# Optimization experiments

Hardware: AMD Instinct MI355X
Metric: run time of the kernel (lower is better)

The kernel has to match this reference:

```python
import jax, jax.numpy as jnp
import numpy as np

PRIME = 2147483647  # 2^31 - 1, MinHash modulus
GAMMA = 0.3
NUM_HEADS = 8


def minhash_sketch(ids, a, b):
    # ids: (B, L, S) int64 atom ids; a,b: (K,) hash coefficients
    # h[b,l,s,k] = (a[k]*id + b[k]) mod PRIME ; signature = min over the set axis S
    h = (ids[..., None] * a + b) % PRIME          # (B, L, S, K)
    return h.min(axis=2)                          # (B, L, K)


def jaccard_from_signatures(sig_q, sig_k):
    # sig_q: (B, Lq, K), sig_k: (B, Lk, K) -> (B, Lq, Lk) fraction of matching slots.
    # Scan over the K hash slots to avoid materializing a (B,Lq,Lk,K) tensor.
    B, Lq, K = sig_q.shape
    Lk = sig_k.shape[1]

    def step(acc, cols):
        qc, kc = cols                              # (B,Lq), (B,Lk)
        return acc + (qc[:, :, None] == kc[:, None, :]).astype(jnp.float32), None

    init = jnp.zeros((B, Lq, Lk), jnp.float32)
    xs = (jnp.moveaxis(sig_q, -1, 0), jnp.moveaxis(sig_k, -1, 0))
    acc, _ = jax.lax.scan(step, init, xs)
    return acc / K


def symdiff_from_jaccard(jacc, size_q, size_k):
    # |A ∩ B| = J/(1+J) * (|A|+|B|)  =>  |A Δ B| = (|A|+|B|) * (1-J)/(1+J)
    tot = size_q[:, :, None] + size_k[:, None, :]   # (B, Lq, Lk)
    return tot * (1.0 - jacc) / (1.0 + jacc)


def setup_inputs() -> dict:
    key = jax.random.key(0)
    ks = jax.random.split(key, 12)
    B, Lq, Lk, E, S, K, V = 4, 1024, 1024, 512, 8, 128, 32000
    w = lambda k: (jax.random.normal(k, (E, E), jnp.float32) * 0.02)
    return {
        "query": jax.random.normal(ks[0], (B, Lq, E), jnp.float32),
        "key": jax.random.normal(ks[1], (B, Lk, E), jnp.float32),
        "value": jax.random.normal(ks[2], (B, Lk, E), jnp.float32),
        "token_sets_q": jax.random.randint(ks[3], (B, Lq, S), 0, V).astype(jnp.int64),
        "token_sets_k": jax.random.randint(ks[4], (B, Lk, S), 0, V).astype(jnp.int64),
        "hash_a": jax.random.randint(ks[5], (K,), 1, PRIME - 1).astype(jnp.int64),
        "hash_b": jax.random.randint(ks[6], (K,), 0, PRIME - 1).astype(jnp.int64),
        "Wq": w(ks[7]), "bq": jnp.zeros((E,), jnp.float32),
        "Wk": w(ks[8]), "bk": jnp.zeros((E,), jnp.float32),
        "Wv": w(ks[9]), "bv": jnp.zeros((E,), jnp.float32),
        "Wo": w(ks[10]), "bo": jnp.zeros((E,), jnp.float32),
    }


def reference(query, key, value, token_sets_q, token_sets_k, hash_a, hash_b,
              Wq, bq, Wk, bk, Wv, bv, Wo, bo):
    B, Lq, E = query.shape
    Lk = key.shape[1]
    H = NUM_HEADS
    d = E // H

    # in-projections (torch Linear: x @ W^T + b); q,k are computed but the
    # attention scores come solely from the token-set kernel (gating disabled)
    q = query @ Wq.T + bq
    k = key @ Wk.T + bk
    v = (value @ Wv.T + bv).reshape(B, Lk, H, d).transpose(0, 2, 1, 3)  # (B,H,Lk,d)

    # MinHash sketches of per-token atom sets -> estimated Jaccard -> Δ-RBF score
    sig_q = minhash_sketch(token_sets_q, hash_a, hash_b)   # (B,Lq,K)
    sig_k = minhash_sketch(token_sets_k, hash_a, hash_b)   # (B,Lk,K)
    jacc = jaccard_from_signatures(sig_q, sig_k)           # (B,Lq,Lk)

    S = token_sets_q.shape[-1]
    size_q = jnp.full((B, Lq), S, jnp.float32)             # uniform CSR offsets -> |set| = S
    size_k = jnp.full((B, Lk), S, jnp.float32)
    delta = symdiff_from_jaccard(jacc, size_q, size_k)
    scores = jnp.exp(-GAMMA * delta)                       # (B,Lq,Lk), shared by all heads

    attn = jax.nn.softmax(scores, axis=-1)                 # no masks, no causal, dropout=0
    ctx = jnp.einsum('bqk,bhkd->bqhd', attn, v).reshape(B, Lq, E)
    return ctx @ Wo.T + bo
```

## Files before the change

### kernel.cpp

```cpp
#include <hip/hip_runtime.h>
#include <hip/hip_bf16.h>
#include <stdint.h>

#define PRIME 2147483647u
#define GAMMA 0.3f
#define K_HASH 128
#define S_SET 8
#define NB 4
#define LQ 1024
#define LK 1024
#define EDIM 512

typedef unsigned short ushort_t;
typedef __attribute__((ext_vector_type(8))) short short8;
typedef __attribute__((ext_vector_type(4))) float f32x4;

static __device__ __forceinline__ unsigned short f2bf(float f) {
    unsigned u = __builtin_bit_cast(unsigned, f);
    u += 0x7FFFu + ((u >> 16) & 1u);
    return (unsigned short)(u >> 16);
}

static __device__ __forceinline__ void glds16(const void* g, void* l) {
    __builtin_amdgcn_global_load_lds(
        (const __attribute__((address_space(1))) unsigned int*)g,
        (__attribute__((address_space(3))) unsigned int*)l, 16, 0, 0);
}

#define SWZ(r) ((((r) >> 2) & 3) ^ ((r) & 3))

static __device__ __forceinline__ float score_of(int m) {
    float r = (float)(K_HASH - m) / (float)(K_HASH + m);
    return expf(expf(-GAMMA * (2.0f * S_SET) * r));
}

template<int SEPI>
static __device__ void gemm64_dev(
        const ushort_t* __restrict__ A, const ushort_t* __restrict__ B,
        ushort_t* __restrict__ C, float* __restrict__ Sacc,
        int lda, int ldb, int ldc, int Kd, int m0, int n0,
        ushort_t* AsBase, ushort_t* BsBase, int tid) {
    ushort_t (*As)[64 * 32] = (ushort_t (*)[64 * 32])AsBase;
    ushort_t (*Bs)[64 * 32] = (ushort_t (*)[64 * 32])BsBase;
    int w = tid >> 6, lane = tid & 63;
    int wm = (w & 1) * 32, wn = (w >> 1) * 32;
    int mrow = lane & 15, kg = lane >> 4;

    int r = tid >> 2, c = (tid & 3) ^ SWZ(r);
    const ushort_t* pa = A + (size_t)(m0 + r) * lda + c * 8;
    const ushort_t* pb = B + (size_t)(n0 + r) * ldb + c * 8;

    int aoff[2], boff[2];
    #pragma unroll
    for (int s = 0; s < 2; s++) {
        int Ra = wm + s * 16 + mrow;
        aoff[s] = Ra * 32 + (kg ^ SWZ(Ra)) * 8;
        int Rb = wn + s * 16 + mrow;
        boff[s] = Rb * 32 + (kg ^ SWZ(Rb)) * 8;
    }

    f32x4 acc[2][2] = {};
    int nK = Kd >> 5;
    glds16(pa, &As[0][tid * 8]);
    glds16(pb, &Bs[0][tid * 8]);
    for (int i = 0; i < nK; i++) {
        __syncthreads();
        int cur = i & 1, nxt = cur ^ 1;
        if (i + 1 < nK) {
            int k0 = (i + 1) << 5;
            glds16(pa + k0, &As[nxt][tid * 8]);
            glds16(pb + k0, &Bs[nxt][tid * 8]);
        }
        short8 af[2], bh[2];
        #pragma unroll
        for (int s = 0; s < 2; s++) {
            af[s] = *(const short8*)&As[cur][aoff[s]];
            bh[s] = *(const short8*)&Bs[cur][boff[s]];
        }
        #pragma unroll
        for (int ii = 0; ii < 2; ii++)
            #pragma unroll
            for (int jj = 0; jj < 2; jj++)
                acc[ii][jj] = __builtin_amdgcn_mfma_f32_16x16x32_bf16(
                                  af[ii], bh[jj], acc[ii][jj], 0, 0, 0);
    }

    int col = lane & 15, rbase = (lane >> 4) * 4;
    #pragma unroll
    for (int ii = 0; ii < 2; ii++) {
        #pragma unroll
        for (int jj = 0; jj < 2; jj++) {
            #pragma unroll
            for (int rr = 0; rr < 4; rr++) {
                int gm = m0 + wm + ii * 16 + rbase + rr;
                int gn = n0 + wn + jj * 16 + col;
                C[(size_t)gm * ldc + gn] = f2bf(acc[ii][jj][rr]);
            }
        }
    }
    if (SEPI) {
        #pragma unroll
        for (int jj = 0; jj < 2; jj++) {
            float s = 0.f;
            #pragma unroll
            for (int ii = 0; ii < 2; ii++)
                #pragma unroll
                for (int rr = 0; rr < 4; rr++) s += acc[ii][jj][rr];
            s += __shfl_xor(s, 16);
            s += __shfl_xor(s, 32);
            if ((lane >> 4) == 0)
                atomicAdd(&Sacc[(m0 >> 10) * EDIM + n0 + wn + jj * 16 + col], s);
        }
    }
}

#define BOB_BLOCKS 8
#define SZ_BLOCKS 1
#define CVT_N0 (NB * LK * EDIM)
#define CVT_N1 (EDIM * EDIM)
#define CVT_BLOCKS ((CVT_N0 + CVT_N1) / (256 * 8))
#define MZ_BLOCKS 1024
#define SIGT_BLOCKS 128
#define WVT_BLOCKS 64
#define PREP_GRID (BOB_BLOCKS + SZ_BLOCKS + CVT_BLOCKS + MZ_BLOCKS + SIGT_BLOCKS + WVT_BLOCKS)

__global__ __launch_bounds__(256) void prep_kernel(
        const float* __restrict__ value, const float* __restrict__ Wv,
        const float* __restrict__ Wo, const float* __restrict__ bv,
        const float* __restrict__ bo,
        ushort_t* __restrict__ Vb, ushort_t* __restrict__ Wob,
        ushort_t* __restrict__ WvT,
        const int* __restrict__ ts_q, const int* __restrict__ ts_k,
        const int* __restrict__ ha, const int* __restrict__ hb,
        unsigned* __restrict__ sigTq, unsigned* __restrict__ sigTk,
        uint8_t* __restrict__ M, float* __restrict__ S,
        float* __restrict__ bob) {
    __shared__ unsigned tile[128 * 65];
    __shared__ int ids_s[64 * S_SET];
    int blk = blockIdx.x, tid = threadIdx.x;
    if (blk < BOB_BLOCKS) {
        int w = tid >> 6, lane = tid & 63;
        #pragma unroll
        for (int i = 0; i < 16; i++) {
            int row = blk * 64 + w * 16 + i;
            const float* wr = Wo + (size_t)row * EDIM;
            float s = 0.f;
            #pragma unroll
            for (int c2 = 0; c2 < 8; c2++)
                s += bv[lane + 64 * c2] * wr[lane + 64 * c2];
            #pragma unroll
            for (int off = 32; off; off >>= 1) s += __shfl_down(s, off);
            if (lane == 0) bob[row] = bo[row] + s;
        }
        return;
    }
    if (blk < BOB_BLOCKS + SZ_BLOCKS) {
        ((float2*)S)[tid] = (float2){0.f, 0.f};
        ((float2*)S)[256 + tid] = (float2){0.f, 0.f};
        ((float2*)S)[512 + tid] = (float2){0.f, 0.f};
        ((float2*)S)[768 + tid] = (float2){0.f, 0.f};
        return;
    }
    if (blk < BOB_BLOCKS + SZ_BLOCKS + CVT_BLOCKS) {
        size_t i = ((size_t)(blk - BOB_BLOCKS - SZ_BLOCKS) * 256 + tid) * 8;
        const float* src; ushort_t* dst; size_t off;
        if (i < CVT_N0) { src = value; dst = Vb;  off = i; }
        else            { src = Wo;    dst = Wob; off = i - CVT_N0; }
        float4 a = *(const float4*)(src + off);
        float4 b = *(const float4*)(src + off + 4);
        ushort4 o0, o1;
        o0.x = f2bf(a.x); o0.y = f2bf(a.y); o0.z = f2bf(a.z); o0.w = f2bf(a.w);
        o1.x = f2bf(b.x); o1.y = f2bf(b.y); o1.z = f2bf(b.z); o1.w = f2bf(b.w);
        *(ushort4*)(dst + off)     = o0;
        *(ushort4*)(dst + off + 4) = o1;
        return;
    }
    if (blk < BOB_BLOCKS + SZ_BLOCKS + CVT_BLOCKS + MZ_BLOCKS) {
        size_t off = ((size_t)(blk - BOB_BLOCKS - SZ_BLOCKS - CVT_BLOCKS) * 256 + tid) * 16;
        *(int4*)(M + off) = (int4){0, 0, 0, 0};
        return;
    }
    if (blk < BOB_BLOCKS + SZ_BLOCKS + CVT_BLOCKS + MZ_BLOCKS + SIGT_BLOCKS) {
        int sb = blk - (BOB_BLOCKS + SZ_BLOCKS + CVT_BLOCKS + MZ_BLOCKS);
        int r0 = sb * 64;
        const int* ts = (r0 < NB * LQ) ? ts_q : ts_k;
        unsigned* sigT = (r0 < NB * LQ) ? sigTq : sigTk;
        int base = r0 & (NB * LQ - 1);
        ((int2*)ids_s)[tid] = ((const int2*)(ts + (size_t)base * S_SET))[tid];
        __syncthreads();
        int kt = tid & 127, rt = tid >> 7;
        unsigned long long a  = (unsigned)ha[kt];
        unsigned long long bb = (unsigned)hb[kt];
        for (int r = rt; r < 64; r += 2) {
            unsigned mn = 0xFFFFFFFFu;
            #pragma unroll
            for (int s = 0; s < S_SET; s++) {
                unsigned long long x =
                    a * (unsigned long long)(unsigned)ids_s[r * S_SET + s] + bb;
                x = (x & PRIME) + (x >> 31);
                x = (x & PRIME) + (x >> 31);
                unsigned rr = (unsigned)x;
                if (rr >= PRIME) rr -= PRIME;
                mn = (rr < mn) ? rr : mn;
            }
            tile[kt * 65 + r] = mn;
        }
        __syncthreads();
        #pragma unroll
        for (int ch = 0; ch < 32; ch++) {
            int idx = ch * 256 + tid;
            int k = idx >> 6, r = idx & 63;
            sigT[(size_t)k * (NB * LQ) + base + r] = tile[k * 65 + r];
        }
        return;
    }
    int wt = blk - (BOB_BLOCKS + SZ_BLOCKS + CVT_BLOCKS + MZ_BLOCKS + SIGT_BLOCKS);
    int r0 = (wt >> 3) * 64, c0 = (wt & 7) * 64;
    ushort_t (*tt)[65] = (ushort_t (*)[65])tile;
    #pragma unroll
    for (int p = 0; p < 16; p++) {
        int idx = p * 256 + tid, r = idx >> 6, c = idx & 63;
        tt[c][r] = f2bf(Wv[(size_t)(r0 + r) * EDIM + c0 + c]);
    }
    __syncthreads();
    #pragma unroll
    for (int p = 0; p < 16; p++) {
        int idx = p * 256 + tid, r = idx >> 6, c = idx & 63;
        WvT[(size_t)(c0 + r) * EDIM + r0 + c] = tt[r][c];
    }
}

union JSmem {
    struct { unsigned keys[2048]; ushort_t vals[2048]; } j;
    struct { ushort_t As[2][64 * 32]; ushort_t Bs[2][64 * 32]; } g;
};

__global__ __launch_bounds__(256) void joing1_kernel(
        const unsigned* __restrict__ sigTq, const unsigned* __restrict__ sigTk,
        uint8_t* __restrict__ M,
        const ushort_t* __restrict__ Wob, const ushort_t* __restrict__ WvT,
        ushort_t* __restrict__ Wvo) {
    __shared__ JSmem sm;
    int blk = blockIdx.x, tid = threadIdx.x;
    if (blk < 64) {
        gemm64_dev<0>(Wob, WvT, Wvo, nullptr,
                      EDIM, EDIM, EDIM, EDIM,
                      (blk >> 3) * 64, (blk & 7) * 64,
                      sm.g.As[0], sm.g.Bs[0], tid);
        return;
    }
    int jt = blk - 64, b = jt >> 7, k = jt & 127;
    const unsigned* kc = sigTk + (size_t)k * (NB * LK) + b * LK;
    const unsigned* qc = sigTq + (size_t)k * (NB * LQ) + b * LQ;
    uint4 kv = ((const uint4*)kc)[tid];
    uint4 qv = ((const uint4*)qc)[tid];
    #pragma unroll
    for (int i = 0; i < 8; i++) sm.j.keys[i * 256 + tid] = 0xFFFFFFFFu;
    __syncthreads();
    unsigned vvv[4] = {kv.x, kv.y, kv.z, kv.w};
    unsigned hh[4]; bool dn[4];
    #pragma unroll
    for (int e = 0; e < 4; e++) { hh[e] = (vvv[e] * 2654435761u) >> 21; dn[e] = false; }
    int rem = 4;
    while (rem) {
        #pragma unroll
        for (int e = 0; e < 4; e++) {
            if (dn[e]) continue;
            unsigned prev = atomicCAS(&sm.j.keys[hh[e]], 0xFFFFFFFFu, vvv[e]);
            if (prev == 0xFFFFFFFFu) {
                sm.j.vals[hh[e]] = (ushort_t)(tid * 4 + e);
                dn[e] = true; rem--;
            } else hh[e] = (hh[e] + 1) & 2047;
        }
    }
    __syncthreads();
    uint8_t* Mb = M + ((size_t)b << 20);
    unsigned qq[4] = {qv.x, qv.y, qv.z, qv.w};
    #pragma unroll
    for (int e = 0; e < 4; e++) { hh[e] = (qq[e] * 2654435761u) >> 21; dn[e] = false; }
    rem = 4;
    while (rem) {
        unsigned kk[4];
        #pragma unroll
        for (int e = 0; e < 4; e++) kk[e] = sm.j.keys[hh[e]];
        #pragma unroll
        for (int e = 0; e < 4; e++) {
            if (dn[e]) continue;
            if (kk[e] == 0xFFFFFFFFu) { dn[e] = true; rem--; }
            else {
                if (kk[e] == qq[e]) {
                    unsigned ix = ((unsigned)(tid * 4 + e) << 10) + sm.j.vals[hh[e]];
                    atomicAdd((unsigned*)(Mb + (ix & ~3u)), 1u << ((ix & 3u) * 8));
                }
                hh[e] = (hh[e] + 1) & 2047;
            }
        }
    }
}

__global__ __launch_bounds__(256) void g2_kernel(
        const ushort_t* __restrict__ Vb, const ushort_t* __restrict__ Wvo,
        ushort_t* __restrict__ W2c, float* __restrict__ S) {
    __shared__ ushort_t As[2][64 * 32], Bs[2][64 * 32];
    int blk = blockIdx.x;
    gemm64_dev<1>(Vb, Wvo, W2c, S,
                  EDIM, EDIM, EDIM, EDIM,
                  (blk >> 3) * 64, (blk & 7) * 64,
                  As[0], Bs[0], threadIdx.x);
}

__global__ __launch_bounds__(256) void outk_kernel(
        const uint8_t* __restrict__ M, const ushort_t* __restrict__ W2c,
        const float* __restrict__ S, const float* __restrict__ bob,
        float* __restrict__ out) {
    __shared__ unsigned lj[256];
    __shared__ float lp[256];
    __shared__ unsigned lcnt;
    int row = blockIdx.x, tid = threadIdx.x, b = row >> 10;
    const uint8_t* Mr = M + ((size_t)row << 10);
    float p0 = score_of(0);
    float acc0 = 0.f, acc1 = 0.f, drs = 0.f;
    int n0 = tid * 2;
    for (int c = 0; c < 4; c++) {
        if (tid == 0) lcnt = 0;
        __syncthreads();
        uint8_t m = Mr[c * 256 + tid];
        if (m) {
            unsigned s = atomicAdd(&lcnt, 1u);
            lj[s] = c * 256 + tid;
            lp[s] = score_of((int)m) - p0;
        }
        __syncthreads();
        unsigned cnt = lcnt;
        for (unsigned i = 0; i < cnt; i++) {
            float w = lp[i];
            drs += w;
            const ushort_t* wr = W2c + (((size_t)(b << 10) + lj[i]) << 9);
            unsigned pk = *(const unsigned*)(wr + n0);
            acc0 += w * __builtin_bit_cast(float, pk << 16);
            acc1 += w * __builtin_bit_cast(float, pk & 0xFFFF0000u);
        }
        __syncthreads();
    }
    float rs = 1024.0f * p0 + drs;
    float inv = 1.0f / rs;
    float2 sv = *(const float2*)(S + b * EDIM + n0);
    float2 bb = *(const float2*)(bob + n0);
    float2 o;
    o.x = (p0 * sv.x + acc0) * inv + bb.x;
    o.y = (p0 * sv.y + acc1) * inv + bb.y;
    *(float2*)(out + (size_t)row * EDIM + n0) = o;
}

extern "C" void kernel_launch(void* const* d_in, const int* in_sizes, int n_in,
                              void* d_out, int out_size, void* d_ws, size_t ws_size,
                              hipStream_t stream) {
    const float* value = (const float*)d_in[2];
    const int* tsq = (const int*)d_in[3];
    const int* tsk = (const int*)d_in[4];
    const int* ha  = (const int*)d_in[5];
    const int* hb  = (const int*)d_in[6];
    const float* Wv = (const float*)d_in[11];
    const float* bv = (const float*)d_in[12];
    const float* Wo = (const float*)d_in[13];
    const float* bo = (const float*)d_in[14];
    float* out = (float*)d_out;

    char* ws = (char*)d_ws;
    unsigned* sigTq = (unsigned*)(ws);
    unsigned* sigTk = (unsigned*)(ws + (2ull << 20));
    uint8_t*  M     = (uint8_t*)(ws + (4ull << 20));
    ushort_t* Vb    = (ushort_t*)(ws + (8ull << 20));
    ushort_t* W2c   = (ushort_t*)(ws + (12ull << 20));
    ushort_t* Wob   = (ushort_t*)(ws + (16ull << 20));
    ushort_t* WvT   = (ushort_t*)(ws + (16ull << 20) + (512ull << 10));
    ushort_t* Wvo   = (ushort_t*)(ws + (17ull << 20));
    float* S        = (float*)(ws + (17ull << 20) + (512ull << 10));
    float* bob      = (float*)(ws + (17ull << 20) + (520ull << 10));

    prep_kernel<<<PREP_GRID, 256, 0, stream>>>(
        value, Wv, Wo, bv, bo, Vb, Wob, WvT,
        tsq, tsk, ha, hb, sigTq, sigTk, M, S, bob);

    joing1_kernel<<<576, 256, 0, stream>>>(
        sigTq, sigTk, M, Wob, WvT, Wvo);

    g2_kernel<<<512, 256, 0, stream>>>(Vb, Wvo, W2c, S);

    outk_kernel<<<NB * LQ, 256, 0, stream>>>(M, W2c, S, bob, out);
}
```

Before: 161.2 us.

## Fuse four kernels into one cooperative persistent kernel with grid syncs

Merges the prep, join/GEMM1, GEMM2 and output kernels into a single 512-block cooperative kernel that runs four phases separated by grid-wide syncs, with a fallback to four separate launches if the cooperative launch fails. Work in each phase is redistributed over 512 persistent blocks (grid-stride loops for conversion/zeroing, multiple rows per block in the output phase). The goal is to remove launch overhead and inter-kernel gaps, at the cost of grid-sync latency, a larger shared-memory union, and less parallelism in the output phase (512 blocks instead of 4096).

```diff
diff --git a/kernel.cpp b/kernel.cpp
--- a/kernel.cpp
+++ b/kernel.cpp
@@ -1,6 +1,9 @@
 #include <hip/hip_runtime.h>
 #include <hip/hip_bf16.h>
+#include <hip/hip_cooperative_groups.h>
 #include <stdint.h>
+
+namespace cg = cooperative_groups;
 
 #define PRIME 2147483647u
 #define GAMMA 0.3f
@@ -33,6 +36,13 @@
     float r = (float)(K_HASH - m) / (float)(K_HASH + m);
     return expf(expf(-GAMMA * (2.0f * S_SET) * r));
 }
+
+union FSmem {
+    struct { unsigned tile[128 * 65]; int ids[64 * S_SET]; } t;
+    struct { unsigned keys[2048]; ushort_t vals[2048]; } j;
+    struct { ushort_t As[2][64 * 32]; ushort_t Bs[2][64 * 32]; } g;
+    struct { unsigned lj[256]; float lp[256]; unsigned lcnt; } o;
+};
 
 template<int SEPI>
 static __device__ void gemm64_dev(
@@ -114,242 +124,232 @@
     }
 }
 
-#define BOB_BLOCKS 8
-#define SZ_BLOCKS 1
 #define CVT_N0 (NB * LK * EDIM)
 #define CVT_N1 (EDIM * EDIM)
-#define CVT_BLOCKS ((CVT_N0 + CVT_N1) / (256 * 8))
-#define MZ_BLOCKS 1024
-#define SIGT_BLOCKS 128
-#define WVT_BLOCKS 64
-#define PREP_GRID (BOB_BLOCKS + SZ_BLOCKS + CVT_BLOCKS + MZ_BLOCKS + SIGT_BLOCKS + WVT_BLOCKS)
-
-__global__ __launch_bounds__(256) void prep_kernel(
+#define CVT_U ((CVT_N0 + CVT_N1) / 8)
+#define MZ_U (NB * LQ * LK / 16)
+#define TOT_U (CVT_U + MZ_U)
+
+__global__ __launch_bounds__(256, 2) void fused_kernel(
         const float* __restrict__ value, const float* __restrict__ Wv,
         const float* __restrict__ Wo, const float* __restrict__ bv,
         const float* __restrict__ bo,
-        ushort_t* __restrict__ Vb, ushort_t* __restrict__ Wob,
-        ushort_t* __restrict__ WvT,
         const int* __restrict__ ts_q, const int* __restrict__ ts_k,
         const int* __restrict__ ha, const int* __restrict__ hb,
         unsigned* __restrict__ sigTq, unsigned* __restrict__ sigTk,
-        uint8_t* __restrict__ M, float* __restrict__ S,
-        float* __restrict__ bob) {
-    __shared__ unsigned tile[128 * 65];
-    __shared__ int ids_s[64 * S_SET];
+        uint8_t* __restrict__ M,
+        ushort_t* __restrict__ Vb, ushort_t* __restrict__ Wob,
+        ushort_t* __restrict__ WvT, ushort_t* __restrict__ Wvo,
+        ushort_t* __restrict__ W2c, float* __restrict__ S,
+        float* __restrict__ bob, float* __restrict__ out,
+        int plo, int phi) {
+    __shared__ FSmem sm;
     int blk = blockIdx.x, tid = threadIdx.x;
-    if (blk < BOB_BLOCKS) {
-        int w = tid >> 6, lane = tid & 63;
-        #pragma unroll
-        for (int i = 0; i < 16; i++) {
-            int row = blk * 64 + w * 16 + i;
-            const float* wr = Wo + (size_t)row * EDIM;
-            float s = 0.f;
-            #pragma unroll
-            for (int c2 = 0; c2 < 8; c2++)
-                s += bv[lane + 64 * c2] * wr[lane + 64 * c2];
-            #pragma unroll
-            for (int off = 32; off; off >>= 1) s += __shfl_down(s, off);
-            if (lane == 0) bob[row] = bo[row] + s;
-        }
-        return;
-    }
-    if (blk < BOB_BLOCKS + SZ_BLOCKS) {
-        ((float2*)S)[tid] = (float2){0.f, 0.f};
-        ((float2*)S)[256 + tid] = (float2){0.f, 0.f};
-        ((float2*)S)[512 + tid] = (float2){0.f, 0.f};
-        ((float2*)S)[768 + tid] = (float2){0.f, 0.f};
-        return;
-    }
-    if (blk < BOB_BLOCKS + SZ_BLOCKS + CVT_BLOCKS) {
-        size_t i = ((size_t)(blk - BOB_BLOCKS - SZ_BLOCKS) * 256 + tid) * 8;
-        const float* src; ushort_t* dst; size_t off;
-        if (i < CVT_N0) { src = value; dst = Vb;  off = i; }
-        else            { src = Wo;    dst = Wob; off = i - CVT_N0; }
-        float4 a = *(const float4*)(src + off);
-        float4 b = *(const float4*)(src + off + 4);
-        ushort4 o0, o1;
-        o0.x = f2bf(a.x); o0.y = f2bf(a.y); o0.z = f2bf(a.z); o0.w = f2bf(a.w);
-        o1.x = f2bf(b.x); o1.y = f2bf(b.y); o1.z = f2bf(b.z); o1.w = f2bf(b.w);
-        *(ushort4*)(dst + off)     = o0;
-        *(ushort4*)(dst + off + 4) = o1;
-        return;
-    }
-    if (blk < BOB_BLOCKS + SZ_BLOCKS + CVT_BLOCKS + MZ_BLOCKS) {
-        size_t off = ((size_t)(blk - BOB_BLOCKS - SZ_BLOCKS - CVT_BLOCKS) * 256 + tid) * 16;
-        *(int4*)(M + off) = (int4){0, 0, 0, 0};
-        return;
-    }
-    if (blk < BOB_BLOCKS + SZ_BLOCKS + CVT_BLOCKS + MZ_BLOCKS + SIGT_BLOCKS) {
-        int sb = blk - (BOB_BLOCKS + SZ_BLOCKS + CVT_BLOCKS + MZ_BLOCKS);
-        int r0 = sb * 64;
-        const int* ts = (r0 < NB * LQ) ? ts_q : ts_k;
-        unsigned* sigT = (r0 < NB * LQ) ? sigTq : sigTk;
-        int base = r0 & (NB * LQ - 1);
-        ((int2*)ids_s)[tid] = ((const int2*)(ts + (size_t)base * S_SET))[tid];
-        __syncthreads();
-        int kt = tid & 127, rt = tid >> 7;
-        unsigned long long a  = (unsigned)ha[kt];
-        unsigned long long bb = (unsigned)hb[kt];
-        for (int r = rt; r < 64; r += 2) {
-            unsigned mn = 0xFFFFFFFFu;
-            #pragma unroll
-            for (int s = 0; s < S_SET; s++) {
-                unsigned long long x =
-                    a * (unsigned long long)(unsigned)ids_s[r * S_SET + s] + bb;
-                x = (x & PRIME) + (x >> 31);
-                x = (x & PRIME) + (x >> 31);
-                unsigned rr = (unsigned)x;
-                if (rr >= PRIME) rr -= PRIME;
-                mn = (rr < mn) ? rr : mn;
+
+    for (int ph = plo; ph <= phi; ph++) {
+        if (ph == 0) {
+            if (blk < 128) {
+                int r0 = blk * 64;
+                const int* ts = (r0 < NB * LQ) ? ts_q : ts_k;
+                unsigned* sigT = (r0 < NB * LQ) ? sigTq : sigTk;
+                int base = r0 & (NB * LQ - 1);
+                ((int2*)sm.t.ids)[tid] =
+                    ((const int2*)(ts + (size_t)base * S_SET))[tid];
+                __syncthreads();
+                int kt = tid & 127, rt = tid >> 7;
+                unsigned long long a  = (unsigned)ha[kt];
+                unsigned long long bb = (unsigned)hb[kt];
+                for (int r = rt; r < 64; r += 2) {
+                    unsigned mn = 0xFFFFFFFFu;
+                    #pragma unroll
+                    for (int s = 0; s < S_SET; s++) {
+                        unsigned long long x =
+                            a * (unsigned long long)(unsigned)sm.t.ids[r * S_SET + s] + bb;
+                        x = (x & PRIME) + (x >> 31);
+                        x = (x & PRIME) + (x >> 31);
+                        unsigned rr = (unsigned)x;
+                        if (rr >= PRIME) rr -= PRIME;
+                        mn = (rr < mn) ? rr : mn;
+                    }
+                    sm.t.tile[kt * 65 + r] = mn;
+                }
+                __syncthreads();
+                #pragma unroll
+                for (int ch = 0; ch < 32; ch++) {
+                    int idx = ch * 256 + tid;
+                    int k = idx >> 6, r = idx & 63;
+                    sigT[(size_t)k * (NB * LQ) + base + r] = sm.t.tile[k * 65 + r];
+                }
+            } else if (blk < 136) {
+                int w = tid >> 6, lane = tid & 63;
+                #pragma unroll
+                for (int i = 0; i < 16; i++) {
+                    int row = (blk - 128) * 64 + w * 16 + i;
+                    const float* wr = Wo + (size_t)row * EDIM;
+                    float s = 0.f;
+                    #pragma unroll
+                    for (int c2 = 0; c2 < 8; c2++)
+                        s += bv[lane + 64 * c2] * wr[lane + 64 * c2];
+                    #pragma unroll
+                    for (int off = 32; off; off >>= 1) s += __shfl_down(s, off);
+                    if (lane == 0) bob[row] = bo[row] + s;
+                }
+            } else if (blk == 136) {
+                #pragma unroll
+                for (int i = 0; i < 4; i++)
+                    ((float4*)S)[i * 256 + tid] = (float4){0.f, 0.f, 0.f, 0.f};
+            } else if (blk < 201) {
+                int wt = blk - 137;
+                int r0 = (wt >> 3) * 64, c0 = (wt & 7) * 64;
+                ushort_t (*tt)[65] = (ushort_t (*)[65])sm.t.tile;
+                #pragma unroll
+                for (int p = 0; p < 16; p++) {
+                    int idx = p * 256 + tid, r = idx >> 6, c = idx & 63;
+                    tt[c][r] = f2bf(Wv[(size_t)(r0 + r) * EDIM + c0 + c]);
+                }
+                __syncthreads();
+                #pragma unroll
+                for (int p = 0; p < 16; p++) {
+                    int idx = p * 256 + tid, r = idx >> 6, c = idx & 63;
+                    WvT[(size_t)(c0 + r) * EDIM + r0 + c] = tt[r][c];
+                }
+            } else {
+                for (size_t u = (size_t)(blk - 201) * 256 + tid; u < TOT_U;
+                     u += (size_t)311 * 256) {
+                    if (u < CVT_U) {
+                        size_t i = u * 8;
+                        const float* src; ushort_t* dst; size_t off;
+                        if (i < CVT_N0) { src = value; dst = Vb;  off = i; }
+                        else            { src = Wo;    dst = Wob; off = i - CVT_N0; }
+                        float4 a = *(const float4*)(src + off);
+                        float4 b = *(const float4*)(src + off + 4);
+                        ushort4 o0, o1;
+                        o0.x = f2bf(a.x); o0.y = f2bf(a.y);
+                        o0.z = f2bf(a.z); o0.w = f2bf(a.w);
+                        o1.x = f2bf(b.x); o1.y = f2bf(b.y);
+                        o1.z = f2bf(b.z); o1.w = f2bf(b.w);
+                        *(ushort4*)(dst + off)     = o0;
+                        *(ushort4*)(dst + off + 4) = o1;
+                    } else {
+                        *(int4*)(M + (u - CVT_U) * 16) = (int4){0, 0, 0, 0};
+                    }
+                }
             }
-            tile[kt * 65 + r] = mn;
-        }
-        __syncthreads();
-        #pragma unroll
-        for (int ch = 0; ch < 32; ch++) {
-            int idx = ch * 256 + tid;
-            int k = idx >> 6, r = idx & 63;
-            sigT[(size_t)k * (NB * LQ) + base + r] = tile[k * 65 + r];
-        }
-        return;
-    }
-    int wt = blk - (BOB_BLOCKS + SZ_BLOCKS + CVT_BLOCKS + MZ_BLOCKS + SIGT_BLOCKS);
-    int r0 = (wt >> 3) * 64, c0 = (wt & 7) * 64;
-    ushort_t (*tt)[65] = (ushort_t (*)[65])tile;
-    #pragma unroll
-    for (int p = 0; p < 16; p++) {
-        int idx = p * 256 + tid, r = idx >> 6, c = idx & 63;
-        tt[c][r] = f2bf(Wv[(size_t)(r0 + r) * EDIM + c0 + c]);
-    }
-    __syncthreads();
-    #pragma unroll
-    for (int p = 0; p < 16; p++) {
-        int idx = p * 256 + tid, r = idx >> 6, c = idx & 63;
-        WvT[(size_t)(c0 + r) * EDIM + r0 + c] = tt[r][c];
-    }
-}
-
-union JSmem {
-    struct { unsigned keys[2048]; ushort_t vals[2048]; } j;
-    struct { ushort_t As[2][64 * 32]; ushort_t Bs[2][64 * 32]; } g;
-};
-
-__global__ __launch_bounds__(256) void joing1_kernel(
-        const unsigned* __restrict__ sigTq, const unsigned* __restrict__ sigTk,
-        uint8_t* __restrict__ M,
-        const ushort_t* __restrict__ Wob, const ushort_t* __restrict__ WvT,
-        ushort_t* __restrict__ Wvo) {
-    __shared__ JSmem sm;
-    int blk = blockIdx.x, tid = threadIdx.x;
-    if (blk < 64) {
-        gemm64_dev<0>(Wob, WvT, Wvo, nullptr,
-                      EDIM, EDIM, EDIM, EDIM,
-                      (blk >> 3) * 64, (blk & 7) * 64,
-                      sm.g.As[0], sm.g.Bs[0], tid);
-        return;
-    }
-    int jt = blk - 64, b = jt >> 7, k = jt & 127;
-    const unsigned* kc = sigTk + (size_t)k * (NB * LK) + b * LK;
-    const unsigned* qc = sigTq + (size_t)k * (NB * LQ) + b * LQ;
-    uint4 kv = ((const uint4*)kc)[tid];
-    uint4 qv = ((const uint4*)qc)[tid];
-    #pragma unroll
-    for (int i = 0; i < 8; i++) sm.j.keys[i * 256 + tid] = 0xFFFFFFFFu;
-    __syncthreads();
-    unsigned vvv[4] = {kv.x, kv.y, kv.z, kv.w};
-    unsigned hh[4]; bool dn[4];
-    #pragma unroll
-    for (int e = 0; e < 4; e++) { hh[e] = (vvv[e] * 2654435761u) >> 21; dn[e] = false; }
-    int rem = 4;
-    while (rem) {
-        #pragma unroll
-        for (int e = 0; e < 4; e++) {
-            if (dn[e]) continue;
-            unsigned prev = atomicCAS(&sm.j.keys[hh[e]], 0xFFFFFFFFu, vvv[e]);
-            if (prev == 0xFFFFFFFFu) {
-                sm.j.vals[hh[e]] = (ushort_t)(tid * 4 + e);
-                dn[e] = true; rem--;
-            } else hh[e] = (hh[e] + 1) & 2047;
-        }
-    }
-    __syncthreads();
-    uint8_t* Mb = M + ((size_t)b << 20);
-    unsigned qq[4] = {qv.x, qv.y, qv.z, qv.w};
-    #pragma unroll
-    for (int e = 0; e < 4; e++) { hh[e] = (qq[e] * 2654435761u) >> 21; dn[e] = false; }
-    rem = 4;
-    while (rem) {
-        unsigned kk[4];
-        #pragma unroll
-        for (int e = 0; e < 4; e++) kk[e] = sm.j.keys[hh[e]];
-        #pragma unroll
-        for (int e = 0; e < 4; e++) {
-            if (dn[e]) continue;
-            if (kk[e] == 0xFFFFFFFFu) { dn[e] = true; rem--; }
-            else {
-                if (kk[e] == qq[e]) {
-                    unsigned ix = ((unsigned)(tid * 4 + e) << 10) + sm.j.vals[hh[e]];
-                    atomicAdd((unsigned*)(Mb + (ix & ~3u)), 1u << ((ix & 3u) * 8));
-                }
-                hh[e] = (hh[e] + 1) & 2047;
+        } else if (ph == 1) {
+            if (blk < 64) {
+                gemm64_dev<0>(Wob, WvT, Wvo, nullptr,
+                              EDIM, EDIM, EDIM, EDIM,
+                              (blk >> 3) * 64, (blk & 7) * 64,
+                              sm.g.As[0], sm.g.Bs[0], tid);
+            } else {
+                for (int u = blk - 64; u < 512; u += 448) {
+                    __syncthreads();
+                    int b = u >> 7, k = u & 127;
+                    const unsigned* kc = sigTk + (size_t)k * (NB * LK) + b * LK;
+                    const unsigned* qc = sigTq + (size_t)k * (NB * LQ) + b * LQ;
+                    uint4 kv = ((const uint4*)kc)[tid];
+                    uint4 qv = ((const uint4*)qc)[tid];
+                    #pragma unroll
+                    for (int i = 0; i < 8; i++)
+                        sm.j.keys[i * 256 + tid] = 0xFFFFFFFFu;
+                    __syncthreads();
+                    unsigned vvv[4] = {kv.x, kv.y, kv.z, kv.w};
+                    unsigned hh[4]; bool dn[4];
+                    #pragma unroll
+                    for (int e = 0; e < 4; e++) {
+                        hh[e] = (vvv[e] * 2654435761u) >> 21; dn[e] = false;
+                    }
+                    int rem = 4;
+                    while (rem) {
+                        #pragma unroll
+                        for (int e = 0; e < 4; e++) {
+                            if (dn[e]) continue;
+                            unsigned prev =
+                                atomicCAS(&sm.j.keys[hh[e]], 0xFFFFFFFFu, vvv[e]);
+                            if (prev == 0xFFFFFFFFu) {
+                                sm.j.vals[hh[e]] = (ushort_t)(tid * 4 + e);
+                                dn[e] = true; rem--;
+                            } else hh[e] = (hh[e] + 1) & 2047;
+                        }
+                    }
+                    __syncthreads();
+                    uint8_t* Mb = M + ((size_t)b << 20);
+                    unsigned qq[4] = {qv.x, qv.y, qv.z, qv.w};
+                    #pragma unroll
+                    for (int e = 0; e < 4; e++) {
+                        hh[e] = (qq[e] * 2654435761u) >> 21; dn[e] = false;
+                    }
+                    rem = 4;
+                    while (rem) {
+                        unsigned kk[4];
+                        #pragma unroll
+                        for (int e = 0; e < 4; e++) kk[e] = sm.j.keys[hh[e]];
+                        #pragma unroll
+                        for (int e = 0; e < 4; e++) {
+                            if (dn[e]) continue;
+                            if (kk[e] == 0xFFFFFFFFu) { dn[e] = true; rem--; }
+                            else {
+                                if (kk[e] == qq[e]) {
+                                    unsigned ix = ((unsigned)(tid * 4 + e) << 10)
+                                                  + sm.j.vals[hh[e]];
+                                    atomicAdd((unsigned*)(Mb + (ix & ~3u)),
+                                              1u << ((ix & 3u) * 8));
+                                }
+                                hh[e] = (hh[e] + 1) & 2047;
+                            }
+                        }
+                    }
+                }
             }
-        }
-    }
-}
-
-__global__ __launch_bounds__(256) void g2_kernel(
-        const ushort_t* __restrict__ Vb, const ushort_t* __restrict__ Wvo,
-        ushort_t* __restrict__ W2c, float* __restrict__ S) {
-    __shared__ ushort_t As[2][64 * 32], Bs[2][64 * 32];
-    int blk = blockIdx.x;
-    gemm64_dev<1>(Vb, Wvo, W2c, S,
-                  EDIM, EDIM, EDIM, EDIM,
-                  (blk >> 3) * 64, (blk & 7) * 64,
-                  As[0], Bs[0], threadIdx.x);
-}
-
-__global__ __launch_bounds__(256) void outk_kernel(
-        const uint8_t* __restrict__ M, const ushort_t* __restrict__ W2c,
-        const float* __restrict__ S, const float* __restrict__ bob,
-        float* __restrict__ out) {
-    __shared__ unsigned lj[256];
-    __shared__ float lp[256];
-    __shared__ unsigned lcnt;
-    int row = blockIdx.x, tid = threadIdx.x, b = row >> 10;
-    const uint8_t* Mr = M + ((size_t)row << 10);
-    float p0 = score_of(0);
-    float acc0 = 0.f, acc1 = 0.f, drs = 0.f;
-    int n0 = tid * 2;
-    for (int c = 0; c < 4; c++) {
-        if (tid == 0) lcnt = 0;
-        __syncthreads();
-        uint8_t m = Mr[c * 256 + tid];
-        if (m) {
-            unsigned s = atomicAdd(&lcnt, 1u);
-            lj[s] = c * 256 + tid;
-            lp[s] = score_of((int)m) - p0;
-        }
-        __syncthreads();
-        unsigned cnt = lcnt;
-        for (unsigned i = 0; i < cnt; i++) {
-            float w = lp[i];
-            drs += w;
-            const ushort_t* wr = W2c + (((size_t)(b << 10) + lj[i]) << 9);
-            unsigned pk = *(const unsigned*)(wr + n0);
-            acc0 += w * __builtin_bit_cast(float, pk << 16);
-            acc1 += w * __builtin_bit_cast(float, pk & 0xFFFF0000u);
-        }
-        __syncthreads();
-    }
-    float rs = 1024.0f * p0 + drs;
-    float inv = 1.0f / rs;
-    float2 sv = *(const float2*)(S + b * EDIM + n0);
-    float2 bb = *(const float2*)(bob + n0);
-    float2 o;
-    o.x = (p0 * sv.x + acc0) * inv + bb.x;
-    o.y = (p0 * sv.y + acc1) * inv + bb.y;
-    *(float2*)(out + (size_t)row * EDIM + n0) = o;
+        } else if (ph == 2) {
+            gemm64_dev<1>(Vb, Wvo, W2c, S,
+                          EDIM, EDIM, EDIM, EDIM,
+                          (blk >> 3) * 64, (blk & 7) * 64,
+                          sm.g.As[0], sm.g.Bs[0], tid);
+        } else {
+            float p0 = score_of(0);
+            for (int it = 0; it < 8; it++) {
+                int row = blk + 512 * it, b = row >> 10;
+                const uint8_t* Mr = M + ((size_t)row << 10);
+                float acc0 = 0.f, acc1 = 0.f, drs = 0.f;
+                int n0 = tid * 2;
+                for (int c = 0; c < 4; c++) {
+                    if (tid == 0) sm.o.lcnt = 0;
+                    __syncthreads();
+                    uint8_t m = Mr[c * 256 + tid];
+                    if (m) {
+                        unsigned s = atomicAdd(&sm.o.lcnt, 1u);
+                        sm.o.lj[s] = c * 256 + tid;
+                        sm.o.lp[s] = score_of((int)m) - p0;
+                    }
+                    __syncthreads();
+                    unsigned cnt = sm.o.lcnt;
+                    for (unsigned i = 0; i < cnt; i++) {
+                        float w = sm.o.lp[i];
+                        drs += w;
+                        const ushort_t* wr =
+                            W2c + (((size_t)(b << 10) + sm.o.lj[i]) << 9);
+                        unsigned pk = *(const unsigned*)(wr + n0);
+                        acc0 += w * __builtin_bit_cast(float, pk << 16);
+                        acc1 += w * __builtin_bit_cast(float, pk & 0xFFFF0000u);
+                    }
+                    __syncthreads();
+                }
+                float rs = 1024.0f * p0 + drs;
+                float inv = 1.0f / rs;
+                float2 sv = *(const float2*)(S + b * EDIM + n0);
+                float2 bb = *(const float2*)(bob + n0);
+                float2 o;
+                o.x = (p0 * sv.x + acc0) * inv + bb.x;
+                o.y = (p0 * sv.y + acc1) * inv + bb.y;
+                *(float2*)(out + (size_t)row * EDIM + n0) = o;
+            }
+        }
+        if (ph < phi) {
+            __threadfence();
+            cg::this_grid().sync();
+        }
+    }
 }
 
 extern "C" void kernel_launch(void* const* d_in, const int* in_sizes, int n_in,
@@ -376,16 +376,23 @@
     ushort_t* WvT   = (ushort_t*)(ws + (16ull << 20) + (512ull << 10));
     ushort_t* Wvo   = (ushort_t*)(ws + (17ull << 20));
     float* S        = (float*)(ws + (17ull << 20) + (512ull << 10));
-    float* bob      = (float*)(ws + (17ull << 20) + (520ull << 10));
-
-    prep_kernel<<<PREP_GRID, 256, 0, stream>>>(
-        value, Wv, Wo, bv, bo, Vb, Wob, WvT,
-        tsq, tsk, ha, hb, sigTq, sigTk, M, S, bob);
-
-    joing1_kernel<<<576, 256, 0, stream>>>(
-        sigTq, sigTk, M, Wob, WvT, Wvo);
-
-    g2_kernel<<<512, 256, 0, stream>>>(Vb, Wvo, W2c, S);
-
-    outk_kernel<<<NB * LQ, 256, 0, stream>>>(M, W2c, S, bob, out);
-}
+    float* bob      = (float*)(ws + (17ull << 20) + (528ull << 10));
+
+    int plo = 0, phi = 3;
+    void* args[] = {
+        (void*)&value, (void*)&Wv, (void*)&Wo, (void*)&bv, (void*)&bo,
+        (void*)&tsq, (void*)&tsk, (void*)&ha, (void*)&hb,
+        (void*)&sigTq, (void*)&sigTk, (void*)&M,
+        (void*)&Vb, (void*)&Wob, (void*)&WvT, (void*)&Wvo,
+        (void*)&W2c, (void*)&S, (void*)&bob, (void*)&out,
+        (void*)&plo, (void*)&phi
+    };
+    hipError_t err = hipLaunchCooperativeKernel(
+        (void*)fused_kernel, dim3(512), dim3(256), args, 0, stream);
+    if (err != hipSuccess) {
+        for (int p = 0; p < 4; p++)
+            fused_kernel<<<512, 256, 0, stream>>>(
+                value, Wv, Wo, bv, bo, tsq, tsk, ha, hb,
+                sigTq, sigTk, M, Vb, Wob, WvT, Wvo, W2c, S, bob, out, p, p);
+    }
+}
```

Result: slower. 546.2 us (+238.9%).
